# Performance work log

Measured on AMD Instinct MI355X. Metric: run time of the kernel, lower is better.

## Reference

```python
import jax, jax.numpy as jnp
import numpy as np

B, S, E = 2, 2048, 2048
H, G = 32, 8          # n_heads, n_groups
D = E // H            # head_dim = 64


def setup_inputs() -> dict:
    key = jax.random.key(0)
    ks = jax.random.split(key, 5)
    scale = 1.0 / np.sqrt(E)
    return {
        "X": jax.random.normal(ks[0], (B, S, E), dtype=jnp.float32),
        "Wq": jax.random.normal(ks[1], (E, E), dtype=jnp.float32) * scale,
        "Wk": jax.random.normal(ks[2], (E, G * D), dtype=jnp.float32) * scale,
        "Wv": jax.random.normal(ks[3], (E, G * D), dtype=jnp.float32) * scale,
        "Wo": jax.random.normal(ks[4], (E, E), dtype=jnp.float32) * scale,
    }


def reference(X, Wq, Wk, Wv, Wo):
    b, s, e = X.shape
    # projections
    q = (X @ Wq).reshape(b, s, H, D).transpose(0, 2, 1, 3)      # [B,H,S,D]
    k = (X @ Wk).reshape(b, s, G, D).transpose(0, 2, 1, 3)      # [B,G,S,D]
    v = (X @ Wv).reshape(b, s, G, D).transpose(0, 2, 1, 3)      # [B,G,S,D]
    # torch view(B, H//G, G, S, D): head h -> (a=h//G, g=h%G)
    q = q.reshape(b, H // G, G, s, D)                           # [B,A,G,S,D]
    scores = jnp.einsum('bagsd,bgtd->bagst', q, k) / np.sqrt(D) # [B,A,G,S,S]
    causal = jnp.tril(jnp.ones((s, s), dtype=bool))
    scores = jnp.where(causal, scores, -jnp.inf)
    probs = jax.nn.softmax(scores, axis=-1)
    out = jnp.einsum('bagst,bgtd->bagsd', probs, v)             # [B,A,G,S,D]
    out = out.reshape(b, H, s, D).transpose(0, 2, 1, 3).reshape(b, s, e)
    return out @ Wo
```

## Files before the change

### kernel.cpp

```cpp
#include <hip/hip_runtime.h>
#include <hip/hip_bf16.h>

typedef unsigned short u16;
typedef __bf16 bf16x8 __attribute__((ext_vector_type(8)));
typedef float f32x4 __attribute__((ext_vector_type(4)));
typedef unsigned short u16x4 __attribute__((ext_vector_type(4)));

#define MFMA16(a, b, c) __builtin_amdgcn_mfma_f32_16x16x32_bf16(a, b, c, 0, 0, 0)

__device__ __forceinline__ u16 f2bf(float f) {
  union { float f; unsigned u; } v; v.f = f;
  unsigned r = v.u + 0x7FFFu + ((v.u >> 16) & 1u);
  return (u16)(r >> 16);
}

__device__ __forceinline__ u16 f2bf_native(float f) {
  __hip_bfloat16 hb = __float2bfloat16(f);
  u16 out;
  __builtin_memcpy(&out, &hb, 2);
  return out;
}

__device__ __forceinline__ void gload16(const u16* g, u16* l) {
  __builtin_amdgcn_global_load_lds(
      (const __attribute__((address_space(1))) unsigned int*)g,
      (__attribute__((address_space(3))) unsigned int*)l, 16, 0, 0);
}

__global__ __launch_bounds__(1024) void preamble(const float* __restrict__ X,
                                                 const float* __restrict__ Wq,
                                                 const float* __restrict__ Wk,
                                                 const float* __restrict__ Wv,
                                                 const float* __restrict__ Wo,
                                                 u16* __restrict__ Xb,
                                                 u16* __restrict__ WqT,
                                                 u16* __restrict__ WkT,
                                                 u16* __restrict__ WvT,
                                                 u16* __restrict__ WoT) {
  const int z = blockIdx.z;
  const int tx = threadIdx.x, ty = threadIdx.y;
  if (z == 4) {
    int bid = blockIdx.y * 64 + blockIdx.x;
    if (bid >= 2048) return;
    int i = bid * 1024 + ty * 32 + tx;
    float4 v = ((const float4*)X)[i];
    u16x4 o = { f2bf(v.x), f2bf(v.y), f2bf(v.z), f2bf(v.w) };
    ((u16x4*)Xb)[i] = o;
    return;
  }
  const float* W; u16* WT; int N;
  if (z == 0)      { W = Wq; WT = WqT; N = 2048; }
  else if (z == 1) { W = Wk; WT = WkT; N = 512; }
  else if (z == 2) { W = Wv; WT = WvT; N = 512; }
  else             { W = Wo; WT = WoT; N = 2048; }
  const int K = 2048;
  int n0 = blockIdx.x * 32;
  if (n0 >= N) return;
  int k0 = blockIdx.y * 32;
  __shared__ float t[32][33];
  t[ty][tx] = W[(size_t)(k0 + ty) * N + n0 + tx];
  __syncthreads();
  WT[(size_t)(n0 + ty) * K + k0 + tx] = f2bf(t[tx][ty]);
}

__device__ __forceinline__ void stage_tile4(const u16* __restrict__ A, const u16* __restrict__ BT,
                                            u16* la, u16* lb, int bm, int bn, int K, int k0, int tid) {
#pragma unroll
  for (int i = 0; i < 2; ++i) {
    int s = i * 256 + tid;
    int row = s >> 2;
    int c = (s & 3) ^ ((row >> 1) & 3);
    gload16(A + (size_t)(bm + row) * K + k0 + c * 8, la + s * 8);
    gload16(BT + (size_t)(bn + row) * K + k0 + c * 8, lb + s * 8);
  }
}

template <int STORE>
__global__ __launch_bounds__(256) void gemm4(const u16* __restrict__ A,
                                             const u16* __restrict__ BT,
                                             void* __restrict__ Cv,
                                             int M, int N, int K) {
  __shared__ u16 lA[2][128 * 32];
  __shared__ u16 lB[2][128 * 32];
  const int tid = threadIdx.x;
  const int lane = tid & 63, wave = tid >> 6;
  const int gx = gridDim.x;
  const int nwg = gx * gridDim.y;
  const int bid = blockIdx.y * gx + blockIdx.x;
  const int sw = (bid & 7) * (nwg >> 3) + (bid >> 3);
  const int bx = sw % gx, by = sw / gx;
  const int bm = by * 128, bn = bx * 128;
  const int wm = (wave >> 1) * 64, wn = (wave & 1) * 64;
  const int l15 = lane & 15, l4 = lane >> 4;

  f32x4 acc[4][4] = {};

  u16* ra = (u16*)lA[0]; u16* rb = (u16*)lB[0];
  u16* wa = (u16*)lA[1]; u16* wb = (u16*)lB[1];

  stage_tile4(A, BT, ra, rb, bm, bn, K, 0, tid);
  asm volatile("s_waitcnt vmcnt(0)" ::: "memory");
  __builtin_amdgcn_s_barrier();

  const int NT = K >> 5;
#pragma unroll 1
  for (int t = 0; t < NT; ++t) {
    if (t + 1 < NT) stage_tile4(A, BT, wa, wb, bm, bn, K, (t + 1) << 5, tid);
    bf16x8 af[4], bf[4];
#pragma unroll
    for (int i = 0; i < 4; ++i) {
      int r = wm + i * 16 + l15;
      af[i] = *(const bf16x8*)&ra[r * 32 + (l4 ^ ((r >> 1) & 3)) * 8];
      int n = wn + i * 16 + l15;
      bf[i] = *(const bf16x8*)&rb[n * 32 + (l4 ^ ((n >> 1) & 3)) * 8];
    }
    __builtin_amdgcn_s_setprio(1);
#pragma unroll
    for (int i = 0; i < 4; ++i)
#pragma unroll
      for (int j = 0; j < 4; ++j)
        acc[i][j] = MFMA16(af[i], bf[j], acc[i][j]);
    __builtin_amdgcn_s_setprio(0);
    asm volatile("s_waitcnt vmcnt(0)" ::: "memory");
    __builtin_amdgcn_s_barrier();
    u16* t1 = ra; ra = wa; wa = t1;
    u16* t2 = rb; rb = wb; wb = t2;
  }

#pragma unroll
  for (int i = 0; i < 4; ++i) {
    int row = bm + wm + i * 16 + l4 * 4;
#pragma unroll
    for (int j = 0; j < 4; ++j) {
      int col = bn + wn + j * 16 + l15;
#pragma unroll
      for (int e = 0; e < 4; ++e) {
        float v = acc[i][j][e];
        if (STORE == 2) {
          ((float*)Cv)[(size_t)(row + e) * N + col] = v;
        } else {
          u16* Qb = (u16*)Cv;
          u16* Kb = Qb + 8388608;
          u16* Vt = Kb + 2097152;
          if (col < 2048)       Qb[(size_t)(row + e) * 2048 + col] = f2bf(v * 0.125f);
          else if (col < 2560)  Kb[(size_t)(row + e) * 512 + (col - 2048)] = f2bf(v);
          else                  Vt[(size_t)(col - 2560) * 4096 + (row + e)] = f2bf(v);
        }
      }
    }
  }
}

__global__ __launch_bounds__(512) void attn_fwd(const u16* __restrict__ Q,
                                                const u16* __restrict__ Kb,
                                                const u16* __restrict__ VT,
                                                u16* __restrict__ AO) {
  const int pair = blockIdx.x, g = blockIdx.y, b = blockIdx.z;
  const int tid = threadIdx.x;
  const int lane = tid & 63;
  const int wave = tid >> 6;
  const int a = wave >> 1;
  const int h = a * 8 + g;
  const int l15 = lane & 15, l4 = lane >> 4;

  __shared__ u16 Klds[2][64 * 64];
  __shared__ u16 Vlds[2][64 * 64];
  __shared__ u16 Plds[8][16 * 64];

  const int srow = tid >> 3, sc = (tid & 7) ^ (srow & 7);

  int cur = 0;
#pragma unroll 1
  for (int pass = 0; pass < 2; ++pass) {
    const int qt = (pass == 0) ? pair : 63 - pair;
    const int qw0 = qt * 32 + (wave & 1) * 16;
    const int nt = qt / 2 + 1;

    const u16* qp = Q + (size_t)(b * 2048 + qw0 + l15) * 2048 + h * 64 + l4 * 8;
    bf16x8 qf0 = *(const bf16x8*)qp;
    bf16x8 qf1 = *(const bf16x8*)(qp + 32);

    float m_r = -1e30f, l_r = 0.f;
    f32x4 o[4] = {};

    {
      gload16(Kb + (size_t)(b * 2048 + 0 + srow) * 512 + g * 64 + sc * 8, &Klds[cur][tid * 8]);
      gload16(VT + (size_t)(g * 64 + srow) * 4096 + b * 2048 + 0 + sc * 8, &Vlds[cur][tid * 8]);
      asm volatile("s_waitcnt vmcnt(0)" ::: "memory");
      __builtin_amdgcn_s_barrier();
    }

#pragma unroll 1
    for (int ti = 0; ti < nt; ++ti) {
      const int t0 = ti * 64;
      if (ti + 1 < nt) {
        const int tn = t0 + 64;
        gload16(Kb + (size_t)(b * 2048 + tn + srow) * 512 + g * 64 + sc * 8, &Klds[cur ^ 1][tid * 8]);
        gload16(VT + (size_t)(g * 64 + srow) * 4096 + b * 2048 + tn + sc * 8, &Vlds[cur ^ 1][tid * 8]);
      }

      if (t0 <= qw0 + 15) {
        const u16* Kc = Klds[cur];
        const u16* Vc = Vlds[cur];
        f32x4 s[4];
        __builtin_amdgcn_s_setprio(1);
#pragma unroll
        for (int ct = 0; ct < 4; ++ct) {
          int t = ct * 16 + l15;
          bf16x8 kf0 = *(const bf16x8*)&Kc[(t * 8 + (l4 ^ (t & 7))) * 8];
          bf16x8 kf1 = *(const bf16x8*)&Kc[(t * 8 + ((l4 + 4) ^ (t & 7))) * 8];
          f32x4 sv = {0.f, 0.f, 0.f, 0.f};
          sv = MFMA16(kf0, qf0, sv);
          sv = MFMA16(kf1, qf1, sv);
          s[ct] = sv;
        }
        __builtin_amdgcn_s_setprio(0);

        if (t0 + 63 > qw0) {
          const int qg = qw0 + l15;
#pragma unroll
          for (int ct = 0; ct < 4; ++ct)
#pragma unroll
            for (int e = 0; e < 4; ++e) {
              int tg = t0 + ct * 16 + l4 * 4 + e;
              if (tg > qg) s[ct][e] = -1e30f;
            }
        }

        float m0 = fmaxf(fmaxf(s[0][0], s[0][1]), fmaxf(s[0][2], s[0][3]));
        float m1 = fmaxf(fmaxf(s[1][0], s[1][1]), fmaxf(s[1][2], s[1][3]));
        float m2 = fmaxf(fmaxf(s[2][0], s[2][1]), fmaxf(s[2][2], s[2][3]));
        float m3 = fmaxf(fmaxf(s[3][0], s[3][1]), fmaxf(s[3][2], s[3][3]));
        float mt = fmaxf(fmaxf(m0, m1), fmaxf(m2, m3));
        mt = fmaxf(mt, __shfl_xor(mt, 16));
        mt = fmaxf(mt, __shfl_xor(mt, 32));

        if (!__all(mt <= m_r + 8.0f)) {
          float mn = fmaxf(m_r, mt);
          float alpha = __expf(m_r - mn);
          m_r = mn;
          l_r *= alpha;
#pragma unroll
          for (int e = 0; e < 4; ++e) {
            float ae = __shfl(alpha, l4 * 4 + e);
            o[0][e] *= ae; o[1][e] *= ae; o[2][e] *= ae; o[3][e] *= ae;
          }
        }

        u16* P = Plds[wave];
        float rs = 0.f;
#pragma unroll
        for (int ct = 0; ct < 4; ++ct) {
          u16x4 pk;
#pragma unroll
          for (int e = 0; e < 4; ++e) {
            float p = __expf(s[ct][e] - m_r);
            rs += p;
            pk[e] = f2bf_native(p);
          }
          int slot = (ct * 2 + (l4 >> 1)) ^ (l15 & 7);
          *(u16x4*)&P[l15 * 64 + slot * 8 + (l4 & 1) * 4] = pk;
        }
        rs += __shfl_xor(rs, 16);
        rs += __shfl_xor(rs, 32);
        l_r += rs;

        __builtin_amdgcn_s_setprio(1);
#pragma unroll
        for (int kk = 0; kk < 2; ++kk) {
          bf16x8 pf = *(const bf16x8*)&P[l15 * 64 + (((kk * 4 + l4) ^ (l15 & 7)) * 8)];
#pragma unroll
          for (int cd = 0; cd < 4; ++cd) {
            int d = cd * 16 + l15;
            bf16x8 vf = *(const bf16x8*)&Vc[(d * 8 + ((kk * 4 + l4) ^ (d & 7))) * 8];
            o[cd] = MFMA16(pf, vf, o[cd]);
          }
        }
        __builtin_amdgcn_s_setprio(0);
      }

      asm volatile("s_waitcnt vmcnt(0)" ::: "memory");
      __builtin_amdgcn_s_barrier();
      cur ^= 1;
    }

    float rli = 1.0f / l_r;
#pragma unroll
    for (int cd = 0; cd < 4; ++cd)
#pragma unroll
      for (int e = 0; e < 4; ++e) {
        float rle = __shfl(rli, l4 * 4 + e);
        int r = l4 * 4 + e;
        int d = cd * 16 + l15;
        AO[(size_t)(b * 2048 + qw0 + r) * 2048 + h * 64 + d] = f2bf_native(o[cd][e] * rle);
      }
  }
}

extern "C" void kernel_launch(void* const* d_in, const int* in_sizes, int n_in,
                              void* d_out, int out_size, void* d_ws, size_t ws_size,
                              hipStream_t stream) {
  const float* X  = (const float*)d_in[0];
  const float* Wq = (const float*)d_in[1];
  const float* Wk = (const float*)d_in[2];
  const float* Wv = (const float*)d_in[3];
  const float* Wo = (const float*)d_in[4];
  float* out = (float*)d_out;

  u16* ws  = (u16*)d_ws;
  u16* Xb  = ws;
  u16* WqT = Xb  + 8388608;
  u16* WkT = WqT + 4194304;
  u16* WvT = WkT + 1048576;
  u16* WoT = WvT + 1048576;
  u16* Qb  = WoT + 4194304;
  u16* Kbf = Qb  + 8388608;
  u16* VTb = Kbf + 2097152;
  u16* AOb = Xb;

  preamble<<<dim3(64, 64, 5), dim3(32, 32), 0, stream>>>(X, Wq, Wk, Wv, Wo,
                                                         Xb, WqT, WkT, WvT, WoT);

  gemm4<4><<<dim3(24, 32), 256, 0, stream>>>(Xb, WqT, Qb, 4096, 3072, 2048);

  attn_fwd<<<dim3(32, 8, 2), 512, 0, stream>>>(Qb, Kbf, VTb, AOb);

  gemm4<2><<<dim3(16, 32), 256, 0, stream>>>(AOb, WoT, out, 4096, 2048, 2048);
}
```

Before: 214.8 us.

## Move Wo transpose-convert into extra attention blocks to overlap with attention

Drops the Wo fp32-to-bf16 transpose from the preamble kernel and runs it in an extra z-slice of the attention grid, 256 blocks each handling 16 tiles through the K shared buffer. The aim is to shorten the serial preamble and hide the Wo conversion behind attention work, which leaves some CUs idle. The risk is that the extra blocks compete with attention blocks for CUs and bandwidth.

```diff
diff --git a/kernel.cpp b/kernel.cpp
--- a/kernel.cpp
+++ b/kernel.cpp
@@ -31,15 +31,13 @@
                                                  const float* __restrict__ Wq,
                                                  const float* __restrict__ Wk,
                                                  const float* __restrict__ Wv,
-                                                 const float* __restrict__ Wo,
                                                  u16* __restrict__ Xb,
                                                  u16* __restrict__ WqT,
                                                  u16* __restrict__ WkT,
-                                                 u16* __restrict__ WvT,
-                                                 u16* __restrict__ WoT) {
+                                                 u16* __restrict__ WvT) {
   const int z = blockIdx.z;
   const int tx = threadIdx.x, ty = threadIdx.y;
-  if (z == 4) {
+  if (z == 3) {
     int bid = blockIdx.y * 64 + blockIdx.x;
     if (bid >= 2048) return;
     int i = bid * 1024 + ty * 32 + tx;
@@ -51,8 +49,7 @@
   const float* W; u16* WT; int N;
   if (z == 0)      { W = Wq; WT = WqT; N = 2048; }
   else if (z == 1) { W = Wk; WT = WkT; N = 512; }
-  else if (z == 2) { W = Wv; WT = WvT; N = 512; }
-  else             { W = Wo; WT = WoT; N = 2048; }
+  else             { W = Wv; WT = WvT; N = 512; }
   const int K = 2048;
   int n0 = blockIdx.x * 32;
   if (n0 >= N) return;
@@ -154,18 +151,39 @@
 __global__ __launch_bounds__(512) void attn_fwd(const u16* __restrict__ Q,
                                                 const u16* __restrict__ Kb,
                                                 const u16* __restrict__ VT,
-                                                u16* __restrict__ AO) {
+                                                u16* __restrict__ AO,
+                                                const float* __restrict__ Wo,
+                                                u16* __restrict__ WoT) {
+  __shared__ u16 Klds[2][64 * 64];
+  __shared__ u16 Vlds[2][64 * 64];
+  __shared__ u16 Plds[8][16 * 64];
+
+  const int tid = threadIdx.x;
+
+  if (blockIdx.z == 2) {
+    float (*ts)[33] = (float (*)[33])Klds;
+    const int tx = tid & 31, ty = tid >> 5;
+    const int bid = blockIdx.y * 32 + blockIdx.x;
+#pragma unroll 1
+    for (int ti = 0; ti < 16; ++ti) {
+      int tile = bid * 16 + ti;
+      int n0 = (tile & 63) * 32, k0 = (tile >> 6) * 32;
+      ts[ty][tx]      = Wo[(size_t)(k0 + ty) * 2048 + n0 + tx];
+      ts[ty + 16][tx] = Wo[(size_t)(k0 + ty + 16) * 2048 + n0 + tx];
+      __syncthreads();
+      WoT[(size_t)(n0 + ty) * 2048 + k0 + tx]      = f2bf(ts[tx][ty]);
+      WoT[(size_t)(n0 + ty + 16) * 2048 + k0 + tx] = f2bf(ts[tx][ty + 16]);
+      __syncthreads();
+    }
+    return;
+  }
+
   const int pair = blockIdx.x, g = blockIdx.y, b = blockIdx.z;
-  const int tid = threadIdx.x;
   const int lane = tid & 63;
   const int wave = tid >> 6;
   const int a = wave >> 1;
   const int h = a * 8 + g;
   const int l15 = lane & 15, l4 = lane >> 4;
-
-  __shared__ u16 Klds[2][64 * 64];
-  __shared__ u16 Vlds[2][64 * 64];
-  __shared__ u16 Plds[8][16 * 64];
 
   const int srow = tid >> 3, sc = (tid & 7) ^ (srow & 7);
 
@@ -318,12 +336,12 @@
   u16* VTb = Kbf + 2097152;
   u16* AOb = Xb;
 
-  preamble<<<dim3(64, 64, 5), dim3(32, 32), 0, stream>>>(X, Wq, Wk, Wv, Wo,
-                                                         Xb, WqT, WkT, WvT, WoT);
+  preamble<<<dim3(64, 64, 4), dim3(32, 32), 0, stream>>>(X, Wq, Wk, Wv,
+                                                         Xb, WqT, WkT, WvT);
 
   gemm4<4><<<dim3(24, 32), 256, 0, stream>>>(Xb, WqT, Qb, 4096, 3072, 2048);
 
-  attn_fwd<<<dim3(32, 8, 2), 512, 0, stream>>>(Qb, Kbf, VTb, AOb);
+  attn_fwd<<<dim3(32, 8, 3), 512, 0, stream>>>(Qb, Kbf, VTb, AOb, Wo, WoT);
 
   gemm4<2><<<dim3(16, 32), 256, 0, stream>>>(AOb, WoT, out, 4096, 2048, 2048);
 }
```

New measurement: 208.9 us (median of 2 runs). 2.8% less time.
